# Performance work log

Hardware: AMD Instinct MI355X
Metric: run time of the kernel (lower is better)

The kernel has to match this reference:

```python
import math
import jax, jax.numpy as jnp
import numpy as np

EPS = 1e-05
_THETA = 180.0 * math.pi / 180.0
COS_T = math.cos(_THETA)   # -1.0
SIN_T = math.sin(_THETA)   # ~1.22e-16 (kept for faithfulness)
FH, FW = 3, 3
SH, SW = 1, 1
PH, PW = 1, 1


def _unfold(x):
    # x: (N, C, H, W) -> patches (N, C*FH*FW, OH, OW), channel-major (c, fh, fw)
    # ordering, matching torch.nn.functional.unfold.
    return jax.lax.conv_general_dilated_patches(
        x, (FH, FW), (SH, SW), [(PH, PH), (PW, PW)])


def _norm(v, axis=-1):
    return jnp.sqrt(jnp.sum(v * v, axis=axis, keepdims=True))


def m_rule(w, x, r, eps):
    # w: (n_filters, in_dim), x: (bs, in_dim), r: (bs, n_filters)
    normalized_w = w / (_norm(w) + eps)                       # (nf, d)
    norm_x = _norm(x) + eps                                   # (bs, 1)
    normalized_x = x / norm_x                                 # (bs, d)
    wx = normalized_x @ normalized_w.T                        # (bs, nf)
    # orth = w_hat - (w_hat . x_hat) x_hat, per (patch, filter) pair
    orth = normalized_w[None, :, :] - wx[:, :, None] * normalized_x[:, None, :]
    normalized_orth = orth / (_norm(orth) + eps)              # (bs, nf, d)
    x_head = (COS_T * normalized_x[:, None, :] + SIN_T * normalized_orth)
    x_head = x_head * norm_x[:, :, None]                      # (bs, nf, d)
    x_diff = x[:, None, :] - x_head                           # (bs, nf, d)
    wx_diff = w[None, :, :] * x_diff                          # (bs, nf, d)
    wx_diff_normalized = wx_diff / (wx_diff.sum(-1, keepdims=True) + eps)
    r_out = wx_diff_normalized * r[:, :, None]                # (bs, nf, d)
    return r_out.sum(1)                                       # (bs, d)


def setup_inputs() -> dict:
    key = jax.random.key(0)
    k1, k2, k3 = jax.random.split(key, 3)
    x = jax.random.normal(k1, (4, 64, 16, 16), dtype=jnp.float32)
    r = jax.random.normal(k2, (4, 128, 16, 16), dtype=jnp.float32)
    weight = jax.random.normal(k3, (128, 64, 3, 3), dtype=jnp.float32) * 0.05
    return {"x": x, "r": r, "weight": weight}


def reference(x, r, weight):
    N, C, H, W = x.shape
    NF = weight.shape[0]
    patches = _unfold(x)                                      # (N, C*9, OH, OW)
    _, IN_DIM, OH, OW = patches.shape
    x_col = patches.reshape(N, IN_DIM, OH * OW).transpose(0, 2, 1).reshape(-1, IN_DIM)
    w_col = weight.reshape(NF, -1)                            # (NF, C*9)
    r_col = r.transpose(0, 2, 3, 1).reshape(-1, NF)           # (N*OH*OW, NF)
    r_new = m_rule(w_col, x_col, r_col, EPS)                  # (N*OH*OW, C*9)
    r_img = r_new.reshape(N, OH * OW, IN_DIM).transpose(0, 2, 1).reshape(N, IN_DIM, OH, OW)
    # F.fold is the linear transpose (adjoint) of unfold: overlapping patches
    # are summed back into the (N, C, H, W) image.
    fold = jax.linear_transpose(_unfold, jax.ShapeDtypeStruct(x.shape, x.dtype))
    return fold(r_img)[0]
```

## Files before the change

kernel.cpp:

```cpp
#include <hip/hip_runtime.h>

constexpr int N  = 4, C = 64, H = 16, W = 16;
constexpr int NF = 128;
constexpr int D  = C * 9;
constexpr float EPSF = 1e-5f;

__global__ void k_prep(const float* __restrict__ w,
                       float* __restrict__ w_t4, float* __restrict__ w2f4) {
    const int o = blockIdx.x * 256 + threadIdx.x;
    if (o >= 73728) return;
    const int j = o & 3;
    {
        const int f = (o >> 2) & 127, k4 = o >> 9;
        w_t4[o] = w[f * D + k4 * 4 + j];
    }
    {
        const int c = (o >> 2) & 63, rest = o >> 8;
        const int ab = rest % 9, fq = rest / 9;
        const int a = ab / 3, b = ab % 3;
        w2f4[o] = w[(fq * 4 + j) * D + c * 9 + (2 - a) * 3 + (2 - b)];
    }
}

__global__ void __launch_bounds__(1024) k_conv_t(
        const float* __restrict__ x, const float4* __restrict__ w_t4,
        const float* __restrict__ r, float* __restrict__ t_g) {
    __shared__ float  xl[C * 24];
    __shared__ double partd[4 * 7 * 128];

    const int bid = blockIdx.x;
    const int ow0 = (bid & 3) * 4;
    const int oh  = (bid >> 2) & 15;
    const int n   = bid >> 6;
    const int tid = threadIdx.x;
    const int f   = tid & 127;
    const int cg  = tid >> 7;

    for (int idx = tid; idx < C * 18; idx += 1024) {
        const int c = idx / 18, rem = idx % 18;
        const int dh = rem / 6, dw = rem % 6;
        const int ih = oh - 1 + dh, iw = ow0 - 1 + dw;
        float v = 0.f;
        if (ih >= 0 && ih < H && iw >= 0 && iw < W)
            v = x[((n * C + c) * H + ih) * W + iw];
        xl[c * 24 + dh * 8 + dw] = v;
    }
    __syncthreads();

    double a0 = 0, a1 = 0, a2 = 0, a3 = 0;
    const int c0 = cg * 8;
    const float4* __restrict__ wp = w_t4 + cg * 18 * 128 + f;

#pragma unroll
    for (int half = 0; half < 2; ++half) {
        float wreg[36];
#pragma unroll
        for (int i = 0; i < 9; ++i) {
            const float4 wv = wp[(half * 9 + i) * 128];
            wreg[i * 4 + 0] = wv.x; wreg[i * 4 + 1] = wv.y;
            wreg[i * 4 + 2] = wv.z; wreg[i * 4 + 3] = wv.w;
        }
#pragma unroll
        for (int cl = 0; cl < 4; ++cl) {
            const int c = c0 + half * 4 + cl;
#pragma unroll
            for (int dh = 0; dh < 3; ++dh) {
                const float* rowp = xl + c * 24 + dh * 8;
                const float4 xa = *(const float4*)rowp;
                const float2 xb = *(const float2*)(rowp + 4);
                double xd[6];
                xd[0] = (double)xa.x; xd[1] = (double)xa.y;
                xd[2] = (double)xa.z; xd[3] = (double)xa.w;
                xd[4] = (double)xb.x; xd[5] = (double)xb.y;
#pragma unroll
                for (int b = 0; b < 3; ++b) {
                    const double wd = (double)wreg[cl * 9 + dh * 3 + b];
                    a0 += wd * xd[b];
                    a1 += wd * xd[b + 1];
                    a2 += wd * xd[b + 2];
                    a3 += wd * xd[b + 3];
                }
            }
        }
    }

    if (cg > 0) {
        partd[(0 * 7 + cg - 1) * 128 + f] = a0;
        partd[(1 * 7 + cg - 1) * 128 + f] = a1;
        partd[(2 * 7 + cg - 1) * 128 + f] = a2;
        partd[(3 * 7 + cg - 1) * 128 + f] = a3;
    }
    __syncthreads();
    if (cg == 0) {
#pragma unroll
        for (int g = 0; g < 7; ++g) {
            a0 += partd[(0 * 7 + g) * 128 + f];
            a1 += partd[(1 * 7 + g) * 128 + f];
            a2 += partd[(2 * 7 + g) * 128 + f];
            a3 += partd[(3 * 7 + g) * 128 + f];
        }
        const int base = ((n * NF + f) * H + oh) * W + ow0;
        const float* rp = r + base;
        float* tp = t_g + base;
        tp[0] = (float)((2.0 * (double)rp[0]) / (2.0 * a0 + (double)EPSF));
        tp[1] = (float)((2.0 * (double)rp[1]) / (2.0 * a1 + (double)EPSF));
        tp[2] = (float)((2.0 * (double)rp[2]) / (2.0 * a2 + (double)EPSF));
        tp[3] = (float)((2.0 * (double)rp[3]) / (2.0 * a3 + (double)EPSF));
    }
}

__global__ void __launch_bounds__(1024) k_convT_out(
        const float* __restrict__ x, const float4* __restrict__ w2f4,
        const float* __restrict__ t_g, float* __restrict__ out) {
    __shared__ float tl[NF * 64];
    __shared__ float fpart[4 * 15 * 64];

    const int bid = blockIdx.x;
    const int w0  = (bid & 3) * 4;
    const int h   = (bid >> 2) & 15;
    const int n   = bid >> 6;
    const int tid = threadIdx.x;
    const int c   = tid & 63;
    const int fg  = tid >> 6;

    for (int idx = tid; idx < NF * 54; idx += 1024) {
        const int ff = idx / 54, rem = idx % 54;
        const int a = rem / 18, ww = rem % 18;
        const int oh2 = h - 1 + a, ow = ww - 1;
        float v = 0.f;
        if (oh2 >= 0 && oh2 < H && ow >= 0 && ow < W)
            v = t_g[((n * NF + ff) * H + oh2) * W + ow];
        tl[ff * 64 + a * 20 + ww] = v;
    }
    __syncthreads();

    float b0 = 0, b1 = 0, b2 = 0, b3 = 0;
#pragma unroll
    for (int q = 0; q < 2; ++q) {
        const int fq = fg * 2 + q;
        const float4* __restrict__ wp = w2f4 + fq * 9 * 64 + c;
        float wq[36];
#pragma unroll
        for (int ab = 0; ab < 9; ++ab) {
            const float4 wv = wp[ab * 64];
            wq[ab * 4 + 0] = wv.x; wq[ab * 4 + 1] = wv.y;
            wq[ab * 4 + 2] = wv.z; wq[ab * 4 + 3] = wv.w;
        }
#pragma unroll
        for (int j = 0; j < 4; ++j) {
            const int fbase = (fq * 4 + j) * 64;
#pragma unroll
            for (int a = 0; a < 3; ++a) {
                const float* rowp = tl + fbase + a * 20 + w0;
                const float4 ta = *(const float4*)rowp;
                const float2 tb = *(const float2*)(rowp + 4);
                const float tw[6] = {ta.x, ta.y, ta.z, ta.w, tb.x, tb.y};
#pragma unroll
                for (int b = 0; b < 3; ++b) {
                    const float wv = wq[(a * 3 + b) * 4 + j];
                    b0 += wv * tw[b];
                    b1 += wv * tw[b + 1];
                    b2 += wv * tw[b + 2];
                    b3 += wv * tw[b + 3];
                }
            }
        }
    }

    if (fg > 0) {
        fpart[(0 * 15 + fg - 1) * 64 + c] = b0;
        fpart[(1 * 15 + fg - 1) * 64 + c] = b1;
        fpart[(2 * 15 + fg - 1) * 64 + c] = b2;
        fpart[(3 * 15 + fg - 1) * 64 + c] = b3;
    }
    __syncthreads();
    if (fg == 0) {
#pragma unroll
        for (int g = 0; g < 15; ++g) {
            b0 += fpart[(0 * 15 + g) * 64 + c];
            b1 += fpart[(1 * 15 + g) * 64 + c];
            b2 += fpart[(2 * 15 + g) * 64 + c];
            b3 += fpart[(3 * 15 + g) * 64 + c];
        }
        const int base = ((n * C + c) * H + h) * W + w0;
        out[base + 0] = x[base + 0] * b0;
        out[base + 1] = x[base + 1] * b1;
        out[base + 2] = x[base + 2] * b2;
        out[base + 3] = x[base + 3] * b3;
    }
}

extern "C" void kernel_launch(void* const* d_in, const int* in_sizes, int n_in,
                              void* d_out, int out_size, void* d_ws, size_t ws_size,
                              hipStream_t stream) {
    const float* x = (const float*)d_in[0];
    const float* r = (const float*)d_in[1];
    const float* w = (const float*)d_in[2];
    float* out = (float*)d_out;

    float* ws    = (float*)d_ws;
    float* w_t4  = ws;
    float* w2f4  = w_t4 + 73728;
    float* t_g   = w2f4 + 73728;

    k_prep<<<288, 256, 0, stream>>>(w, w_t4, w2f4);
    k_conv_t<<<256, 1024, 0, stream>>>(x, (const float4*)w_t4, r, t_g);
    k_convT_out<<<256, 1024, 0, stream>>>(x, (const float4*)w2f4, t_g, out);
}
```

Measured before the change: 74.68 us.

## Retile conv kernels to 8 outputs per thread and split filters/channels across blocks

Both convolution kernels now compute 8 adjacent output columns per thread instead of 4, and split the filter (or channel) dimension across two blocks. Each thread therefore loads its weights once and reuses them over more outputs, and the input halo overhead per output shrinks. The cross-thread reduction is parallelized across 512/256 threads instead of being done serially by one group. In exchange each thread needs more accumulator registers (doubles in the first kernel), and the reduction takes more shared-memory passes.

```diff
diff --git a/kernel.cpp b/kernel.cpp
--- a/kernel.cpp
+++ b/kernel.cpp
@@ -25,168 +25,159 @@
 __global__ void __launch_bounds__(1024) k_conv_t(
         const float* __restrict__ x, const float4* __restrict__ w_t4,
         const float* __restrict__ r, float* __restrict__ t_g) {
-    __shared__ float  xl[C * 24];
-    __shared__ double partd[4 * 7 * 128];
+    __shared__ float  xl[C * 36];
+    __shared__ double partd[16 * 8 * 64];
 
     const int bid = blockIdx.x;
-    const int ow0 = (bid & 3) * 4;
+    const int fh  = bid & 1;
+    const int ow0 = ((bid >> 1) & 1) * 8;
     const int oh  = (bid >> 2) & 15;
     const int n   = bid >> 6;
     const int tid = threadIdx.x;
-    const int f   = tid & 127;
-    const int cg  = tid >> 7;
-
-    for (int idx = tid; idx < C * 18; idx += 1024) {
-        const int c = idx / 18, rem = idx % 18;
-        const int dh = rem / 6, dw = rem % 6;
+    const int f   = tid & 63;
+    const int cg  = tid >> 6;
+
+    for (int idx = tid; idx < C * 30; idx += 1024) {
+        const int c = idx / 30, rem = idx % 30;
+        const int dh = rem / 10, dw = rem % 10;
         const int ih = oh - 1 + dh, iw = ow0 - 1 + dw;
         float v = 0.f;
         if (ih >= 0 && ih < H && iw >= 0 && iw < W)
             v = x[((n * C + c) * H + ih) * W + iw];
-        xl[c * 24 + dh * 8 + dw] = v;
-    }
-    __syncthreads();
-
-    double a0 = 0, a1 = 0, a2 = 0, a3 = 0;
-    const int c0 = cg * 8;
-    const float4* __restrict__ wp = w_t4 + cg * 18 * 128 + f;
-
-#pragma unroll
-    for (int half = 0; half < 2; ++half) {
-        float wreg[36];
-#pragma unroll
-        for (int i = 0; i < 9; ++i) {
-            const float4 wv = wp[(half * 9 + i) * 128];
-            wreg[i * 4 + 0] = wv.x; wreg[i * 4 + 1] = wv.y;
-            wreg[i * 4 + 2] = wv.z; wreg[i * 4 + 3] = wv.w;
-        }
-#pragma unroll
-        for (int cl = 0; cl < 4; ++cl) {
-            const int c = c0 + half * 4 + cl;
-#pragma unroll
-            for (int dh = 0; dh < 3; ++dh) {
-                const float* rowp = xl + c * 24 + dh * 8;
-                const float4 xa = *(const float4*)rowp;
-                const float2 xb = *(const float2*)(rowp + 4);
-                double xd[6];
-                xd[0] = (double)xa.x; xd[1] = (double)xa.y;
-                xd[2] = (double)xa.z; xd[3] = (double)xa.w;
-                xd[4] = (double)xb.x; xd[5] = (double)xb.y;
-#pragma unroll
-                for (int b = 0; b < 3; ++b) {
-                    const double wd = (double)wreg[cl * 9 + dh * 3 + b];
-                    a0 += wd * xd[b];
-                    a1 += wd * xd[b + 1];
-                    a2 += wd * xd[b + 2];
-                    a3 += wd * xd[b + 3];
-                }
+        xl[c * 36 + dh * 12 + dw] = v;
+    }
+    __syncthreads();
+
+    const int c0 = cg * 4;
+    const float4* __restrict__ wp = w_t4 + (cg * 9) * 128 + fh * 64 + f;
+
+    float wreg[36];
+#pragma unroll
+    for (int i = 0; i < 9; ++i) {
+        const float4 wv = wp[i * 128];
+        wreg[i * 4 + 0] = wv.x; wreg[i * 4 + 1] = wv.y;
+        wreg[i * 4 + 2] = wv.z; wreg[i * 4 + 3] = wv.w;
+    }
+
+    double acc[8];
+#pragma unroll
+    for (int o = 0; o < 8; ++o) acc[o] = 0.0;
+
+#pragma unroll
+    for (int cl = 0; cl < 4; ++cl) {
+#pragma unroll
+        for (int dh = 0; dh < 3; ++dh) {
+            const float* rowp = xl + (c0 + cl) * 36 + dh * 12;
+            const float4 xa = *(const float4*)rowp;
+            const float4 xb = *(const float4*)(rowp + 4);
+            const float2 xc = *(const float2*)(rowp + 8);
+            double xd[10];
+            xd[0] = (double)xa.x; xd[1] = (double)xa.y;
+            xd[2] = (double)xa.z; xd[3] = (double)xa.w;
+            xd[4] = (double)xb.x; xd[5] = (double)xb.y;
+            xd[6] = (double)xb.z; xd[7] = (double)xb.w;
+            xd[8] = (double)xc.x; xd[9] = (double)xc.y;
+#pragma unroll
+            for (int b = 0; b < 3; ++b) {
+                const double wd = (double)wreg[cl * 9 + dh * 3 + b];
+#pragma unroll
+                for (int o = 0; o < 8; ++o)
+                    acc[o] += wd * xd[b + o];
             }
         }
     }
 
-    if (cg > 0) {
-        partd[(0 * 7 + cg - 1) * 128 + f] = a0;
-        partd[(1 * 7 + cg - 1) * 128 + f] = a1;
-        partd[(2 * 7 + cg - 1) * 128 + f] = a2;
-        partd[(3 * 7 + cg - 1) * 128 + f] = a3;
-    }
-    __syncthreads();
-    if (cg == 0) {
-#pragma unroll
-        for (int g = 0; g < 7; ++g) {
-            a0 += partd[(0 * 7 + g) * 128 + f];
-            a1 += partd[(1 * 7 + g) * 128 + f];
-            a2 += partd[(2 * 7 + g) * 128 + f];
-            a3 += partd[(3 * 7 + g) * 128 + f];
-        }
-        const int base = ((n * NF + f) * H + oh) * W + ow0;
-        const float* rp = r + base;
-        float* tp = t_g + base;
-        tp[0] = (float)((2.0 * (double)rp[0]) / (2.0 * a0 + (double)EPSF));
-        tp[1] = (float)((2.0 * (double)rp[1]) / (2.0 * a1 + (double)EPSF));
-        tp[2] = (float)((2.0 * (double)rp[2]) / (2.0 * a2 + (double)EPSF));
-        tp[3] = (float)((2.0 * (double)rp[3]) / (2.0 * a3 + (double)EPSF));
+#pragma unroll
+    for (int o = 0; o < 8; ++o)
+        partd[(cg * 8 + o) * 64 + f] = acc[o];
+    __syncthreads();
+
+    if (tid < 512) {
+        const int f2 = tid & 63, o = tid >> 6;
+        double s = 0.0;
+#pragma unroll
+        for (int g = 0; g < 16; ++g)
+            s += partd[(g * 8 + o) * 64 + f2];
+        const int fglob = fh * 64 + f2;
+        const int idx = ((n * NF + fglob) * H + oh) * W + ow0 + o;
+        t_g[idx] = (float)((2.0 * (double)r[idx]) / (2.0 * s + (double)EPSF));
     }
 }
 
 __global__ void __launch_bounds__(1024) k_convT_out(
         const float* __restrict__ x, const float4* __restrict__ w2f4,
         const float* __restrict__ t_g, float* __restrict__ out) {
-    __shared__ float tl[NF * 64];
-    __shared__ float fpart[4 * 15 * 64];
+    __shared__ float tl[NF * 36];
+    __shared__ float fpart[32 * 8 * 32];
 
     const int bid = blockIdx.x;
-    const int w0  = (bid & 3) * 4;
+    const int ch  = bid & 1;
+    const int w0  = ((bid >> 1) & 1) * 8;
     const int h   = (bid >> 2) & 15;
     const int n   = bid >> 6;
     const int tid = threadIdx.x;
-    const int c   = tid & 63;
-    const int fg  = tid >> 6;
-
-    for (int idx = tid; idx < NF * 54; idx += 1024) {
-        const int ff = idx / 54, rem = idx % 54;
-        const int a = rem / 18, ww = rem % 18;
-        const int oh2 = h - 1 + a, ow = ww - 1;
+    const int c   = tid & 31;
+    const int fg  = tid >> 5;
+
+    for (int idx = tid; idx < NF * 30; idx += 1024) {
+        const int ff = idx / 30, rem = idx % 30;
+        const int a = rem / 10, ww = rem % 10;
+        const int oh2 = h - 1 + a, ow = w0 - 1 + ww;
         float v = 0.f;
         if (oh2 >= 0 && oh2 < H && ow >= 0 && ow < W)
             v = t_g[((n * NF + ff) * H + oh2) * W + ow];
-        tl[ff * 64 + a * 20 + ww] = v;
-    }
-    __syncthreads();
-
-    float b0 = 0, b1 = 0, b2 = 0, b3 = 0;
-#pragma unroll
-    for (int q = 0; q < 2; ++q) {
-        const int fq = fg * 2 + q;
-        const float4* __restrict__ wp = w2f4 + fq * 9 * 64 + c;
-        float wq[36];
-#pragma unroll
-        for (int ab = 0; ab < 9; ++ab) {
-            const float4 wv = wp[ab * 64];
-            wq[ab * 4 + 0] = wv.x; wq[ab * 4 + 1] = wv.y;
-            wq[ab * 4 + 2] = wv.z; wq[ab * 4 + 3] = wv.w;
-        }
-#pragma unroll
-        for (int j = 0; j < 4; ++j) {
-            const int fbase = (fq * 4 + j) * 64;
-#pragma unroll
-            for (int a = 0; a < 3; ++a) {
-                const float* rowp = tl + fbase + a * 20 + w0;
-                const float4 ta = *(const float4*)rowp;
-                const float2 tb = *(const float2*)(rowp + 4);
-                const float tw[6] = {ta.x, ta.y, ta.z, ta.w, tb.x, tb.y};
-#pragma unroll
-                for (int b = 0; b < 3; ++b) {
-                    const float wv = wq[(a * 3 + b) * 4 + j];
-                    b0 += wv * tw[b];
-                    b1 += wv * tw[b + 1];
-                    b2 += wv * tw[b + 2];
-                    b3 += wv * tw[b + 3];
-                }
+        tl[ff * 36 + a * 12 + ww] = v;
+    }
+    __syncthreads();
+
+    const float4* __restrict__ wp = w2f4 + (fg * 9) * 64 + ch * 32 + c;
+    float wq[36];
+#pragma unroll
+    for (int ab = 0; ab < 9; ++ab) {
+        const float4 wv = wp[ab * 64];
+        wq[ab * 4 + 0] = wv.x; wq[ab * 4 + 1] = wv.y;
+        wq[ab * 4 + 2] = wv.z; wq[ab * 4 + 3] = wv.w;
+    }
+
+    float acc[8];
+#pragma unroll
+    for (int o = 0; o < 8; ++o) acc[o] = 0.f;
+
+#pragma unroll
+    for (int j = 0; j < 4; ++j) {
+        const int fi = fg * 4 + j;
+#pragma unroll
+        for (int a = 0; a < 3; ++a) {
+            const float* rowp = tl + fi * 36 + a * 12;
+            const float4 ta = *(const float4*)rowp;
+            const float4 tb = *(const float4*)(rowp + 4);
+            const float2 tc = *(const float2*)(rowp + 8);
+            const float tw[10] = {ta.x, ta.y, ta.z, ta.w,
+                                  tb.x, tb.y, tb.z, tb.w, tc.x, tc.y};
+#pragma unroll
+            for (int b = 0; b < 3; ++b) {
+                const float wv = wq[(a * 3 + b) * 4 + j];
+#pragma unroll
+                for (int o = 0; o < 8; ++o)
+                    acc[o] += wv * tw[b + o];
             }
         }
     }
 
-    if (fg > 0) {
-        fpart[(0 * 15 + fg - 1) * 64 + c] = b0;
-        fpart[(1 * 15 + fg - 1) * 64 + c] = b1;
-        fpart[(2 * 15 + fg - 1) * 64 + c] = b2;
-        fpart[(3 * 15 + fg - 1) * 64 + c] = b3;
-    }
-    __syncthreads();
-    if (fg == 0) {
-#pragma unroll
-        for (int g = 0; g < 15; ++g) {
-            b0 += fpart[(0 * 15 + g) * 64 + c];
-            b1 += fpart[(1 * 15 + g) * 64 + c];
-            b2 += fpart[(2 * 15 + g) * 64 + c];
-            b3 += fpart[(3 * 15 + g) * 64 + c];
-        }
-        const int base = ((n * C + c) * H + h) * W + w0;
-        out[base + 0] = x[base + 0] * b0;
-        out[base + 1] = x[base + 1] * b1;
-        out[base + 2] = x[base + 2] * b2;
-        out[base + 3] = x[base + 3] * b3;
+#pragma unroll
+    for (int o = 0; o < 8; ++o)
+        fpart[(fg * 8 + o) * 32 + c] = acc[o];
+    __syncthreads();
+
+    if (tid < 256) {
+        const int c2 = tid & 31, o = tid >> 5;
+        float s = 0.f;
+#pragma unroll
+        for (int g = 0; g < 32; ++g)
+            s += fpart[(g * 8 + o) * 32 + c2];
+        const int cglob = ch * 32 + c2;
+        const int idx = ((n * C + cglob) * H + h) * W + w0 + o;
+        out[idx] = x[idx] * s;
     }
 }
 
```

Measured after the change: 71.90 us. 3.7% less time.
